# Optimization experiments

Measured on AMD Instinct MI355X. Metric: run time of the kernel, lower is better.

## Reference

```python
import jax, jax.numpy as jnp
import numpy as np

IN_FEATURES = 4096
OUT_FEATURES = 8192
PADDED = 8192  # 2**ceil(log2(out_features))


def fwht(x):
    """Fast Walsh-Hadamard transform over last axis (n power of 2), normalized by 1/sqrt(n)."""
    orig_shape = x.shape
    n = orig_shape[-1]
    h = x.reshape(-1, n)
    step = 1
    while step < n:  # static loop, log2(n) iterations
        h = h.reshape(-1, n // (2 * step), 2, step)
        a = h[:, :, 0, :]
        b = h[:, :, 1, :]
        h = jnp.stack([a + b, a - b], axis=2).reshape(-1, n)
        step *= 2
    return (h * (1.0 / np.sqrt(n)).astype(np.float32)).reshape(orig_shape)


def setup_inputs() -> dict:
    key = jax.random.key(0)
    kx, kb, kg, kp = jax.random.split(key, 4)
    x = jax.random.normal(kx, (8192, IN_FEATURES), dtype=jnp.float32)
    B = jnp.where(jax.random.uniform(kb, (PADDED,)) < 0.5, -1.0, 1.0).astype(jnp.float32)
    G = jax.random.normal(kg, (PADDED,), dtype=jnp.float32)
    perm = jax.random.permutation(kp, PADDED).astype(jnp.int32)
    return {"x": x, "B": B, "G": G, "perm": perm}


def reference(x, B, G, perm):
    lead = x.shape[:-1]
    flat = x.reshape(-1, IN_FEATURES)
    pad_len = PADDED - IN_FEATURES
    if pad_len > 0:
        flat = jnp.pad(flat, ((0, 0), (0, pad_len)))
    out = flat * B[None, :]
    out = fwht(out)
    out = out[:, perm]
    out = out * G[None, :]
    out = fwht(out)
    out = out[:, :OUT_FEATURES]
    return out.reshape(*lead, OUT_FEATURES)
```

## Files before the change

### kernel.cpp

```cpp
#include <hip/hip_runtime.h>


constexpr int N  = 8192;
constexpr int NT = 256;
constexpr int NR = 32;
constexpr int LDS_WORDS = N + 2 * (N / 32);

__device__ __forceinline__ int padw(int w) { return w + 2 * (w >> 5); }

template <int FIRST_MASK>
__device__ __forceinline__ void butterfly(float v[NR]) {
    #pragma unroll
    for (int b = FIRST_MASK; b < NR; b <<= 1) {
        #pragma unroll
        for (int r = 0; r < NR; ++r) {
            if ((r & b) == 0) {
                float a = v[r], c = v[r ^ b];
                v[r]     = a + c;
                v[r ^ b] = a - c;
            }
        }
    }
}

__global__ __launch_bounds__(NT) void fastfood_kernel(
    const float* __restrict__ x, const float* __restrict__ Bv,
    const float* __restrict__ Gv, const int* __restrict__ perm,
    float* __restrict__ out)
{
    __shared__ float lds[LDS_WORDS];
    const int t = threadIdx.x;
    const int row = blockIdx.x;
    const float* xrow = x + (size_t)row * 4096;
    float v[NR];

    #pragma unroll
    for (int m = 0; m < 8; ++m) {
        int j = m * 512 + 2 * t;
        float2 xv = *(const float2*)(xrow + j);
        float2 bv = *(const float2*)(Bv + j);
        v[2 * m]     = xv.x * bv.x;
        v[2 * m + 1] = xv.y * bv.y;
    }
    #pragma unroll
    for (int m = 8; m < 16; ++m) { v[2 * m] = 0.f; v[2 * m + 1] = 0.f; }

    butterfly<1>(v);
    #pragma unroll
    for (int m = 0; m < 16; ++m) {
        int w = m * 512 + 2 * t;
        *(float2*)&lds[padw(w)] = make_float2(v[2 * m], v[2 * m + 1]);
    }
    __syncthreads();
    #pragma unroll
    for (int m = 0; m < 16; ++m) {
        int w = t * 32 + 2 * m;
        float2 d = *(const float2*)&lds[padw(w)];
        v[2 * m] = d.x; v[2 * m + 1] = d.y;
    }
    butterfly<2>(v);
    __syncthreads();
    #pragma unroll
    for (int m = 0; m < 16; ++m) {
        int w = t * 32 + 2 * m;
        *(float2*)&lds[padw(w)] = make_float2(v[2 * m], v[2 * m + 1]);
    }
    __syncthreads();
    #pragma unroll
    for (int m = 0; m < 16; ++m) {
        int w = (t >> 4) * 512 + m * 32 + (t & 15) * 2;
        float2 d = *(const float2*)&lds[padw(w)];
        v[2 * m] = d.x; v[2 * m + 1] = d.y;
    }
    butterfly<2>(v);
    __syncthreads();
    #pragma unroll
    for (int m = 0; m < 16; ++m) {
        int w = (t >> 4) * 512 + m * 32 + (t & 15) * 2;
        *(float2*)&lds[padw(w)] = make_float2(v[2 * m], v[2 * m + 1]);
    }
    __syncthreads();

    const float scale = 1.0f / 8192.0f;
    #pragma unroll
    for (int m = 0; m < 16; ++m) {
        int j = m * 512 + 2 * t;
        int2 q = *(const int2*)(perm + j);
        float2 g = *(const float2*)(Gv + j);
        v[2 * m]     = lds[q.x + 2 * (q.x >> 5)] * g.x * scale;
        v[2 * m + 1] = lds[q.y + 2 * (q.y >> 5)] * g.y * scale;
    }

    butterfly<1>(v);
    __syncthreads();
    #pragma unroll
    for (int m = 0; m < 16; ++m) {
        int w = m * 512 + 2 * t;
        *(float2*)&lds[padw(w)] = make_float2(v[2 * m], v[2 * m + 1]);
    }
    __syncthreads();
    #pragma unroll
    for (int m = 0; m < 16; ++m) {
        int w = t * 32 + 2 * m;
        float2 d = *(const float2*)&lds[padw(w)];
        v[2 * m] = d.x; v[2 * m + 1] = d.y;
    }
    butterfly<2>(v);
    __syncthreads();
    #pragma unroll
    for (int m = 0; m < 16; ++m) {
        int w = t * 32 + 2 * m;
        *(float2*)&lds[padw(w)] = make_float2(v[2 * m], v[2 * m + 1]);
    }
    __syncthreads();
    #pragma unroll
    for (int m = 0; m < 16; ++m) {
        int w = (t >> 4) * 512 + m * 32 + (t & 15) * 2;
        float2 d = *(const float2*)&lds[padw(w)];
        v[2 * m] = d.x; v[2 * m + 1] = d.y;
    }
    butterfly<2>(v);

    float* orow = out + (size_t)row * 8192;
    #pragma unroll
    for (int m = 0; m < 16; ++m) {
        int j = (t >> 4) * 512 + m * 32 + (t & 15) * 2;
        *(float2*)(orow + j) = make_float2(v[2 * m], v[2 * m + 1]);
    }
}

extern "C" void kernel_launch(void* const* d_in, const int* in_sizes, int n_in,
                              void* d_out, int out_size, void* d_ws, size_t ws_size,
                              hipStream_t stream) {
    const float* x    = (const float*)d_in[0];
    const float* Bv   = (const float*)d_in[1];
    const float* Gv   = (const float*)d_in[2];
    const int*   perm = (const int*)d_in[3];
    float* out = (float*)d_out;
    fastfood_kernel<<<dim3(8192), dim3(NT), 0, stream>>>(x, Bv, Gv, perm, out);
}
```

Measured before the change: 386.7 us.

## Remove redundant barriers, prefetch perm, reorder FWHT layouts, raise occupancy hint

Drops the barrier between each butterfly and its matching LDS write-back wherever a thread writes the same addresses it just read, which cuts the number of __syncthreads per row. The permutation indices are loaded early into registers so the gather can start right after the barrier. The layout after the permuted gather and the final output layout are swapped, so results are written with a contiguous per-thread stride, and the 1/N scale is moved to the final store. launch_bounds now requests 4 blocks per CU, which may raise register pressure or cause spills because of the q[16] array.

Result: faster. 377.9 us (-2.3%).

```diff
diff --git a/kernel.cpp b/kernel.cpp
--- a/kernel.cpp
+++ b/kernel.cpp
@@ -23,7 +23,7 @@
     }
 }
 
-__global__ __launch_bounds__(NT) void fastfood_kernel(
+__global__ __launch_bounds__(NT, 4) void fastfood_kernel(
     const float* __restrict__ x, const float* __restrict__ Bv,
     const float* __restrict__ Gv, const int* __restrict__ perm,
     float* __restrict__ out)
@@ -32,11 +32,16 @@
     const int t = threadIdx.x;
     const int row = blockIdx.x;
     const float* xrow = x + (size_t)row * 4096;
+
+    const int wA = 2 * t;
+    const int wB = t * 32;
+    const int wC = (t >> 4) * 512 + (t & 15) * 2;
+
     float v[NR];
 
     #pragma unroll
     for (int m = 0; m < 8; ++m) {
-        int j = m * 512 + 2 * t;
+        int j = m * 512 + wA;
         float2 xv = *(const float2*)(xrow + j);
         float2 bv = *(const float2*)(Bv + j);
         v[2 * m]     = xv.x * bv.x;
@@ -47,85 +52,74 @@
 
     butterfly<1>(v);
     #pragma unroll
-    for (int m = 0; m < 16; ++m) {
-        int w = m * 512 + 2 * t;
-        *(float2*)&lds[padw(w)] = make_float2(v[2 * m], v[2 * m + 1]);
-    }
+    for (int m = 0; m < 16; ++m)
+        *(float2*)&lds[padw(m * 512 + wA)] = make_float2(v[2 * m], v[2 * m + 1]);
     __syncthreads();
+
     #pragma unroll
     for (int m = 0; m < 16; ++m) {
-        int w = t * 32 + 2 * m;
-        float2 d = *(const float2*)&lds[padw(w)];
+        float2 d = *(const float2*)&lds[padw(wB + 2 * m)];
         v[2 * m] = d.x; v[2 * m + 1] = d.y;
     }
     butterfly<2>(v);
+    #pragma unroll
+    for (int m = 0; m < 16; ++m)
+        *(float2*)&lds[padw(wB + 2 * m)] = make_float2(v[2 * m], v[2 * m + 1]);
     __syncthreads();
+
     #pragma unroll
     for (int m = 0; m < 16; ++m) {
-        int w = t * 32 + 2 * m;
-        *(float2*)&lds[padw(w)] = make_float2(v[2 * m], v[2 * m + 1]);
+        float2 d = *(const float2*)&lds[padw(wC + m * 32)];
+        v[2 * m] = d.x; v[2 * m + 1] = d.y;
     }
+    int2 q[16];
+    #pragma unroll
+    for (int m = 0; m < 16; ++m)
+        q[m] = *(const int2*)(perm + wC + m * 32);
+    butterfly<2>(v);
+    #pragma unroll
+    for (int m = 0; m < 16; ++m)
+        *(float2*)&lds[padw(wC + m * 32)] = make_float2(v[2 * m], v[2 * m + 1]);
     __syncthreads();
+
     #pragma unroll
     for (int m = 0; m < 16; ++m) {
-        int w = (t >> 4) * 512 + m * 32 + (t & 15) * 2;
-        float2 d = *(const float2*)&lds[padw(w)];
-        v[2 * m] = d.x; v[2 * m + 1] = d.y;
-    }
-    butterfly<2>(v);
-    __syncthreads();
-    #pragma unroll
-    for (int m = 0; m < 16; ++m) {
-        int w = (t >> 4) * 512 + m * 32 + (t & 15) * 2;
-        *(float2*)&lds[padw(w)] = make_float2(v[2 * m], v[2 * m + 1]);
-    }
-    __syncthreads();
-
-    const float scale = 1.0f / 8192.0f;
-    #pragma unroll
-    for (int m = 0; m < 16; ++m) {
-        int j = m * 512 + 2 * t;
-        int2 q = *(const int2*)(perm + j);
-        float2 g = *(const float2*)(Gv + j);
-        v[2 * m]     = lds[q.x + 2 * (q.x >> 5)] * g.x * scale;
-        v[2 * m + 1] = lds[q.y + 2 * (q.y >> 5)] * g.y * scale;
+        float2 g = *(const float2*)(Gv + wC + m * 32);
+        v[2 * m]     = lds[q[m].x + 2 * (q[m].x >> 5)] * g.x;
+        v[2 * m + 1] = lds[q[m].y + 2 * (q[m].y >> 5)] * g.y;
     }
 
     butterfly<1>(v);
     __syncthreads();
     #pragma unroll
-    for (int m = 0; m < 16; ++m) {
-        int w = m * 512 + 2 * t;
-        *(float2*)&lds[padw(w)] = make_float2(v[2 * m], v[2 * m + 1]);
-    }
+    for (int m = 0; m < 16; ++m)
+        *(float2*)&lds[padw(wC + m * 32)] = make_float2(v[2 * m], v[2 * m + 1]);
     __syncthreads();
+
     #pragma unroll
     for (int m = 0; m < 16; ++m) {
-        int w = t * 32 + 2 * m;
-        float2 d = *(const float2*)&lds[padw(w)];
+        float2 d = *(const float2*)&lds[padw(wB + 2 * m)];
         v[2 * m] = d.x; v[2 * m + 1] = d.y;
     }
     butterfly<2>(v);
+    #pragma unroll
+    for (int m = 0; m < 16; ++m)
+        *(float2*)&lds[padw(wB + 2 * m)] = make_float2(v[2 * m], v[2 * m + 1]);
     __syncthreads();
+
     #pragma unroll
     for (int m = 0; m < 16; ++m) {
-        int w = t * 32 + 2 * m;
-        *(float2*)&lds[padw(w)] = make_float2(v[2 * m], v[2 * m + 1]);
-    }
-    __syncthreads();
-    #pragma unroll
-    for (int m = 0; m < 16; ++m) {
-        int w = (t >> 4) * 512 + m * 32 + (t & 15) * 2;
-        float2 d = *(const float2*)&lds[padw(w)];
+        float2 d = *(const float2*)&lds[padw(m * 512 + wA)];
         v[2 * m] = d.x; v[2 * m + 1] = d.y;
     }
     butterfly<2>(v);
 
+    const float scale = 1.0f / 8192.0f;
     float* orow = out + (size_t)row * 8192;
     #pragma unroll
     for (int m = 0; m < 16; ++m) {
-        int j = (t >> 4) * 512 + m * 32 + (t & 15) * 2;
-        *(float2*)(orow + j) = make_float2(v[2 * m], v[2 * m + 1]);
+        int j = m * 512 + wA;
+        *(float2*)(orow + j) = make_float2(v[2 * m] * scale, v[2 * m + 1] * scale);
     }
 }
 
```
